# Performance work log

Hardware: AMD Instinct MI355X
Metric: run time of the kernel (lower is better)

The kernel has to match this reference:

```python
import jax, jax.numpy as jnp
import numpy as np


def setup_inputs() -> dict:
    key = jax.random.key(0)
    k1, k2, k3 = jax.random.split(key, 3)
    B = 8388608
    x = jax.random.normal(k1, (B, 3), dtype=jnp.float32)
    # fc1: Linear(6, 4) -> weight [4, 6], bias [4]
    W = jax.random.normal(k2, (4, 6), dtype=jnp.float32) * (1.0 / jnp.sqrt(6.0))
    b = jax.random.normal(k3, (4,), dtype=jnp.float32) * 0.1
    return {"x": x, "W": W, "b": b}


def softsign(v):
    return v / (1.0 + jnp.abs(v))


def reference(x, W, b):
    angles = x[:, 2:3]                       # [B, 1]
    ones = jnp.ones_like(angles)
    feat = jnp.concatenate((x, jnp.sin(angles), jnp.cos(angles), ones), axis=1)  # [B, 6]
    h = feat @ W.T + b                       # [B, 4]
    out_angles = jnp.arctan2(softsign(h[:, 2:3]), softsign(h[:, 3:4]))  # [B, 1]
    return jnp.concatenate((h[:, :2], out_angles), axis=1)  # [B, 3]
```

## Files before the change

kernel.cpp:

```cpp
#include <hip/hip_runtime.h>
#include <math.h>


__global__ __launch_bounds__(256) void net_main_kernel(
    const float4* __restrict__ x4,
    const float*  __restrict__ W,
    const float*  __restrict__ bias,
    float4*       __restrict__ o4,
    int nquad)
{
    const int t = blockIdx.x * blockDim.x + threadIdx.x;
    if (t >= nquad) return;

    float w[4][5];
    float wb[4];
#pragma unroll
    for (int r = 0; r < 4; ++r) {
#pragma unroll
        for (int c = 0; c < 5; ++c) w[r][c] = W[r * 6 + c];
        wb[r] = W[r * 6 + 5] + bias[r];
    }

    const float4 qa = x4[3 * t + 0];
    const float4 qb = x4[3 * t + 1];
    const float4 qc = x4[3 * t + 2];

    const float rx[4][3] = {
        {qa.x, qa.y, qa.z},
        {qa.w, qb.x, qb.y},
        {qb.z, qb.w, qc.x},
        {qc.y, qc.z, qc.w},
    };

    float res[4][3];
#pragma unroll
    for (int i = 0; i < 4; ++i) {
        const float x0 = rx[i][0];
        const float x1 = rx[i][1];
        const float an = rx[i][2];
        const float s = __sinf(an);
        const float c = __cosf(an);

        float h[4];
#pragma unroll
        for (int r = 0; r < 4; ++r) {
            float acc = wb[r];
            acc = fmaf(c,  w[r][4], acc);
            acc = fmaf(s,  w[r][3], acc);
            acc = fmaf(an, w[r][2], acc);
            acc = fmaf(x1, w[r][1], acc);
            acc = fmaf(x0, w[r][0], acc);
            h[r] = acc;
        }

        const float ss2 = h[2] / (1.0f + fabsf(h[2]));
        const float ss3 = h[3] / (1.0f + fabsf(h[3]));

        res[i][0] = h[0];
        res[i][1] = h[1];
        res[i][2] = atan2f(ss2, ss3);
    }

    o4[3 * t + 0] = make_float4(res[0][0], res[0][1], res[0][2], res[1][0]);
    o4[3 * t + 1] = make_float4(res[1][1], res[1][2], res[2][0], res[2][1]);
    o4[3 * t + 2] = make_float4(res[2][2], res[3][0], res[3][1], res[3][2]);
}

__global__ void net_tail_kernel(
    const float* __restrict__ x,
    const float* __restrict__ W,
    const float* __restrict__ bias,
    float*       __restrict__ out,
    int row0, int nrows)
{
    const int i = blockIdx.x * blockDim.x + threadIdx.x;
    if (i >= nrows) return;
    const int row = row0 + i;

    const float x0 = x[row * 3 + 0];
    const float x1 = x[row * 3 + 1];
    const float an = x[row * 3 + 2];
    const float s = __sinf(an);
    const float c = __cosf(an);

    float h[4];
#pragma unroll
    for (int r = 0; r < 4; ++r) {
        float acc = W[r * 6 + 5] + bias[r];
        acc = fmaf(c,  W[r * 6 + 4], acc);
        acc = fmaf(s,  W[r * 6 + 3], acc);
        acc = fmaf(an, W[r * 6 + 2], acc);
        acc = fmaf(x1, W[r * 6 + 1], acc);
        acc = fmaf(x0, W[r * 6 + 0], acc);
        h[r] = acc;
    }
    const float ss2 = h[2] / (1.0f + fabsf(h[2]));
    const float ss3 = h[3] / (1.0f + fabsf(h[3]));
    out[row * 3 + 0] = h[0];
    out[row * 3 + 1] = h[1];
    out[row * 3 + 2] = atan2f(ss2, ss3);
}

extern "C" void kernel_launch(void* const* d_in, const int* in_sizes, int n_in,
                              void* d_out, int out_size, void* d_ws, size_t ws_size,
                              hipStream_t stream) {
    const float* x    = (const float*)d_in[0];
    const float* W    = (const float*)d_in[1];
    const float* bias = (const float*)d_in[2];
    float* out        = (float*)d_out;

    const int B = in_sizes[0] / 3;
    const int nquad = B / 4;
    const int tail_rows = B - nquad * 4;

    if (nquad > 0) {
        const int block = 256;
        const int grid = (nquad + block - 1) / block;
        net_main_kernel<<<grid, block, 0, stream>>>(
            (const float4*)x, W, bias, (float4*)out, nquad);
    }
    if (tail_rows > 0) {
        net_tail_kernel<<<1, 64, 0, stream>>>(x, W, bias, out, nquad * 4, tail_rows);
    }
}
```

Before: 42.68 us.

## Use polynomial atan2, drop softsign divides, process eight rows per thread

Replaces the library atan2f with a minimax polynomial approximation that uses a hardware reciprocal. The two softsign divisions are removed by cross-multiplying, since atan2 depends only on the ratio and the positive denominators do not change the signs. Each thread now handles eight rows with six float4 loads and stores instead of four, and launch bounds request higher occupancy. These cut the ALU cost of the transcendental and divides in a memory-bound kernel, at the price of approximation error in the angle output and more registers per thread.

```diff
diff --git a/kernel.cpp b/kernel.cpp
--- a/kernel.cpp
+++ b/kernel.cpp
@@ -2,15 +2,31 @@
 #include <math.h>
 
 
-__global__ __launch_bounds__(256) void net_main_kernel(
+__device__ __forceinline__ float fast_atan2f(float y, float x) {
+    const float ax = fabsf(x), ay = fabsf(y);
+    const float mx = fmaxf(ax, ay), mn = fminf(ax, ay);
+    float r = mn * __builtin_amdgcn_rcpf(mx);
+    const float t = r * r;
+    float p = fmaf(t, -0.0851330f, 0.1801410f);
+    p = fmaf(t, p, -0.3302995f);
+    p = fmaf(t, p, 0.9998660f);
+    float a = r * p;
+    a = (ay > ax)   ? (1.57079632679f - a) : a;
+    a = (x < 0.0f)  ? (3.14159265359f - a) : a;
+    a = copysignf(a, y);
+    a = (mx == 0.0f) ? 0.0f : a;
+    return a;
+}
+
+__global__ __launch_bounds__(256, 8) void net_main_kernel(
     const float4* __restrict__ x4,
     const float*  __restrict__ W,
     const float*  __restrict__ bias,
     float4*       __restrict__ o4,
-    int nquad)
+    int ngrp)
 {
     const int t = blockIdx.x * blockDim.x + threadIdx.x;
-    if (t >= nquad) return;
+    if (t >= ngrp) return;
 
     float w[4][5];
     float wb[4];
@@ -21,23 +37,23 @@
         wb[r] = W[r * 6 + 5] + bias[r];
     }
 
-    const float4 qa = x4[3 * t + 0];
-    const float4 qb = x4[3 * t + 1];
-    const float4 qc = x4[3 * t + 2];
+    float4 q[6];
+#pragma unroll
+    for (int i = 0; i < 6; ++i) q[i] = x4[6 * t + i];
 
-    const float rx[4][3] = {
-        {qa.x, qa.y, qa.z},
-        {qa.w, qb.x, qb.y},
-        {qb.z, qb.w, qc.x},
-        {qc.y, qc.z, qc.w},
-    };
+    float f[24];
+#pragma unroll
+    for (int i = 0; i < 6; ++i) {
+        f[4 * i + 0] = q[i].x; f[4 * i + 1] = q[i].y;
+        f[4 * i + 2] = q[i].z; f[4 * i + 3] = q[i].w;
+    }
 
-    float res[4][3];
+    float g[24];
 #pragma unroll
-    for (int i = 0; i < 4; ++i) {
-        const float x0 = rx[i][0];
-        const float x1 = rx[i][1];
-        const float an = rx[i][2];
+    for (int i = 0; i < 8; ++i) {
+        const float x0 = f[3 * i + 0];
+        const float x1 = f[3 * i + 1];
+        const float an = f[3 * i + 2];
         const float s = __sinf(an);
         const float c = __cosf(an);
 
@@ -53,17 +69,16 @@
             h[r] = acc;
         }
 
-        const float ss2 = h[2] / (1.0f + fabsf(h[2]));
-        const float ss3 = h[3] / (1.0f + fabsf(h[3]));
-
-        res[i][0] = h[0];
-        res[i][1] = h[1];
-        res[i][2] = atan2f(ss2, ss3);
+        g[3 * i + 0] = h[0];
+        g[3 * i + 1] = h[1];
+        g[3 * i + 2] = fast_atan2f(h[2] * (1.0f + fabsf(h[3])),
+                                   h[3] * (1.0f + fabsf(h[2])));
     }
 
-    o4[3 * t + 0] = make_float4(res[0][0], res[0][1], res[0][2], res[1][0]);
-    o4[3 * t + 1] = make_float4(res[1][1], res[1][2], res[2][0], res[2][1]);
-    o4[3 * t + 2] = make_float4(res[2][2], res[3][0], res[3][1], res[3][2]);
+#pragma unroll
+    for (int i = 0; i < 6; ++i)
+        o4[6 * t + i] = make_float4(g[4 * i + 0], g[4 * i + 1],
+                                    g[4 * i + 2], g[4 * i + 3]);
 }
 
 __global__ void net_tail_kernel(
@@ -94,11 +109,10 @@
         acc = fmaf(x0, W[r * 6 + 0], acc);
         h[r] = acc;
     }
-    const float ss2 = h[2] / (1.0f + fabsf(h[2]));
-    const float ss3 = h[3] / (1.0f + fabsf(h[3]));
     out[row * 3 + 0] = h[0];
     out[row * 3 + 1] = h[1];
-    out[row * 3 + 2] = atan2f(ss2, ss3);
+    out[row * 3 + 2] = fast_atan2f(h[2] * (1.0f + fabsf(h[3])),
+                                   h[3] * (1.0f + fabsf(h[2])));
 }
 
 extern "C" void kernel_launch(void* const* d_in, const int* in_sizes, int n_in,
@@ -110,16 +124,16 @@
     float* out        = (float*)d_out;
 
     const int B = in_sizes[0] / 3;
-    const int nquad = B / 4;
-    const int tail_rows = B - nquad * 4;
+    const int ngrp = B / 8;
+    const int tail_rows = B - ngrp * 8;
 
-    if (nquad > 0) {
+    if (ngrp > 0) {
         const int block = 256;
-        const int grid = (nquad + block - 1) / block;
+        const int grid = (ngrp + block - 1) / block;
         net_main_kernel<<<grid, block, 0, stream>>>(
-            (const float4*)x, W, bias, (float4*)out, nquad);
+            (const float4*)x, W, bias, (float4*)out, ngrp);
     }
     if (tail_rows > 0) {
-        net_tail_kernel<<<1, 64, 0, stream>>>(x, W, bias, out, nquad * 4, tail_rows);
+        net_tail_kernel<<<1, 64, 0, stream>>>(x, W, bias, out, ngrp * 8, tail_rows);
     }
 }
```

New measurement: 58.53 us. 37.1% more time.
